# Optimization experiments

Measured on AMD Instinct MI355X. Metric: run time of the kernel, lower is better.

The kernel has to match this reference:

```python
import jax, jax.numpy as jnp
import numpy as np

HEADS = 10
DIM_HEAD = 64
C = 640
N_TOK = 1024          # (1024//32)**2 tokens per image
IMG_NUMS = 3          # total_length = id_length + 1
ID_LENGTH = 2
SA = 0.5
NEG_INF = -1e9


def _build_story_mask(key):
    # Faithful to cal_attn_mask_xl: one random row of columns shared by all
    # images, columns beyond the id_length reference images zeroed, and each
    # image's own block forced True; then broadcast over query tokens.
    L = IMG_NUMS * N_TOK
    base = jax.random.uniform(key, (1, L)) < SA                  # [1, L]
    bm = jnp.tile(base, (IMG_NUMS, 1))                           # [img, L]
    col = jnp.arange(L)
    bm = jnp.where(col[None, :] >= ID_LENGTH * N_TOK, False, bm)
    self_block = (col // N_TOK)[None, :] == jnp.arange(IMG_NUMS)[:, None]
    bm = bm | self_block                                         # [img, L]
    return jnp.repeat(bm, N_TOK, axis=0)                         # [L, L]


def setup_inputs() -> dict:
    key = jax.random.key(0)
    ks = jax.random.split(key, 7)
    B_total = 2 * IMG_NUMS
    hidden_states = jax.random.normal(ks[0], (B_total, N_TOK, C), dtype=jnp.float32)
    mask = _build_story_mask(ks[1])
    s = 1.0 / np.sqrt(C)
    Wq = jax.random.normal(ks[2], (C, HEADS * DIM_HEAD), dtype=jnp.float32) * s
    Wk = jax.random.normal(ks[3], (C, HEADS * DIM_HEAD), dtype=jnp.float32) * s
    Wv = jax.random.normal(ks[4], (C, HEADS * DIM_HEAD), dtype=jnp.float32) * s
    Wout = jax.random.normal(ks[5], (HEADS * DIM_HEAD, C), dtype=jnp.float32) * s
    bout = jnp.zeros((C,), dtype=jnp.float32)
    return {"hidden_states": hidden_states, "mask": mask,
            "Wq": Wq, "Wk": Wk, "Wv": Wv, "Wout": Wout, "bout": bout}


def reference(hidden_states, mask, Wq, Wk, Wv, Wout, bout):
    # __call1__ with encoder_hidden_states=None: fuse img_nums images into one
    # long sequence per CFG branch, then masked SDPA.
    B_total, n_tok, c = hidden_states.shape
    img_nums = B_total // 2
    L = img_nums * n_tok
    x = hidden_states.reshape(2, L, c)                       # [2, L, C]

    q = jnp.einsum('bsc,cd->bsd', x, Wq).reshape(2, L, HEADS, DIM_HEAD)
    k = jnp.einsum('bsc,cd->bsd', x, Wk).reshape(2, L, HEADS, DIM_HEAD)
    v = jnp.einsum('bsc,cd->bsd', x, Wv).reshape(2, L, HEADS, DIM_HEAD)

    scale = 1.0 / jnp.sqrt(jnp.asarray(DIM_HEAD, dtype=q.dtype))
    scores = jnp.einsum('bqhd,bkhd->bhqk', q, k) * scale     # [2, H, L, L]
    scores = jnp.where(mask[None, None, :, :], scores, NEG_INF)
    attn = jax.nn.softmax(scores, axis=-1)
    out = jnp.einsum('bhqk,bkhd->bqhd', attn, v)             # [2, L, H, Dh]
    out = out.reshape(B_total, n_tok, HEADS * DIM_HEAD)
    return jnp.einsum('bsd,dc->bsc', out, Wout) + bout
```

## Files before the change

### kernel.cpp

```cpp
#include <hip/hip_runtime.h>
#include <cstdint>
#include <cstddef>

typedef _Float16 f16;
typedef _Float16 f16x8 __attribute__((ext_vector_type(8)));
typedef _Float16 f16x4 __attribute__((ext_vector_type(4)));
typedef float f32x4 __attribute__((ext_vector_type(4)));

#define MFMA32(a, b, c) __builtin_amdgcn_mfma_f32_16x16x32_f16((a), (b), (c), 0, 0, 0)
#define MFMA16(a, b, c) __builtin_amdgcn_mfma_f32_16x16x16f16((a), (b), (c), 0, 0, 0)

#if __has_builtin(__builtin_amdgcn_exp2f)
#define EXP2F(x) __builtin_amdgcn_exp2f(x)
#else
#define EXP2F(x) exp2f(x)
#endif

#define DRAIN_MEM() __builtin_amdgcn_s_waitcnt(0x0070)

#define LOG2E 1.44269504088896340736f

__device__ __forceinline__ f16x4 pack4(float a, float b, float c, float d) {
    f16x4 r; r[0] = (f16)a; r[1] = (f16)b; r[2] = (f16)c; r[3] = (f16)d;
    return r;
}

__device__ __forceinline__ void gl_lds16(const f16* g, f16* l) {
    __builtin_amdgcn_global_load_lds((const __attribute__((address_space(1))) void*)g,
                                     (__attribute__((address_space(3))) void*)l, 16, 0, 0);
}

__global__ __launch_bounds__(256) void k_cvt_x(const float4* __restrict__ x, f16x4* __restrict__ xb) {
    const int i = blockIdx.x * 256 + threadIdx.x;
    const float4 v = x[i];
    f16x4 o;
    o[0] = (f16)v.x; o[1] = (f16)v.y; o[2] = (f16)v.z; o[3] = (f16)v.w;
    xb[i] = o;
}

__global__ __launch_bounds__(256) void k_cvt_w(const float* __restrict__ Wq, const float* __restrict__ Wk,
                                               const float* __restrict__ Wv, const float* __restrict__ Wo,
                                               f16* __restrict__ WT, f16* __restrict__ WoT) {
    __shared__ float tile[32][33];
    const int z = blockIdx.z;
    const float* src = (z == 0) ? Wq : (z == 1) ? Wk : (z == 2) ? Wv : Wo;
    f16* dst = (z < 3) ? (WT + (size_t)z * 640 * 640) : WoT;
    const float scale = (z == 0) ? 0.125f * LOG2E : 1.0f;
    const int k0 = blockIdx.x * 32, n0 = blockIdx.y * 32;
    const int t = threadIdx.x;
#pragma unroll
    for (int i = 0; i < 4; i++) {
        const int idx = i * 256 + t;
        const int r = idx >> 5, c = idx & 31;
        tile[r][c] = src[(size_t)(k0 + r) * 640 + n0 + c];
    }
    __syncthreads();
#pragma unroll
    for (int i = 0; i < 4; i++) {
        const int idx = i * 256 + t;
        const int r = idx >> 5, c = idx & 31;
        dst[(size_t)(n0 + r) * 640 + k0 + c] = (f16)(tile[c][r] * scale);
    }
}

__global__ __launch_bounds__(256) void k_gemm(const f16* __restrict__ A, const f16* __restrict__ B,
                                              f16* __restrict__ qb, f16* __restrict__ kb, f16* __restrict__ vtb) {
    __shared__ f16 As[128 * 40];
    __shared__ f16 Bs[128 * 40];
    const int t = threadIdx.x;
    const int wave = t >> 6, lane = t & 63, quad = lane >> 4, l16 = lane & 15;
    const int wm = wave >> 1, wn = wave & 1;
    const long m0 = (long)blockIdx.x * 128, n0 = (long)blockIdx.y * 128;
    const int srow = t >> 2, skc = t & 3;

    const f32x4 zero = {0.f, 0.f, 0.f, 0.f};
    f32x4 acc[4][4];
#pragma unroll
    for (int i = 0; i < 4; i++)
#pragma unroll
        for (int j = 0; j < 4; j++) acc[i][j] = zero;

    const f16* gA1 = A + (m0 + srow) * 640 + skc * 8;
    const f16* gA2 = A + (m0 + 64 + srow) * 640 + skc * 8;
    const f16* gB1 = B + (n0 + srow) * 640 + skc * 8;
    const f16* gB2 = B + (n0 + 64 + srow) * 640 + skc * 8;
    f16* sA1 = As + srow * 40 + skc * 8;
    f16* sA2 = As + (64 + srow) * 40 + skc * 8;
    f16* sB1 = Bs + srow * 40 + skc * 8;
    f16* sB2 = Bs + (64 + srow) * 40 + skc * 8;

    for (int kt = 0; kt < 20; kt++) {
        const int ko = kt * 32;
        const f16x8 a1 = *(const f16x8*)(gA1 + ko);
        const f16x8 a2 = *(const f16x8*)(gA2 + ko);
        const f16x8 b1 = *(const f16x8*)(gB1 + ko);
        const f16x8 b2 = *(const f16x8*)(gB2 + ko);
        __syncthreads();
        *(f16x8*)sA1 = a1;
        *(f16x8*)sA2 = a2;
        *(f16x8*)sB1 = b1;
        *(f16x8*)sB2 = b2;
        __syncthreads();
        f16x8 af[4], bfr[4];
#pragma unroll
        for (int mi = 0; mi < 4; mi++) af[mi] = *(const f16x8*)(As + (wm * 64 + mi * 16 + l16) * 40 + quad * 8);
#pragma unroll
        for (int ni = 0; ni < 4; ni++) bfr[ni] = *(const f16x8*)(Bs + (wn * 64 + ni * 16 + l16) * 40 + quad * 8);
#pragma unroll
        for (int mi = 0; mi < 4; mi++)
#pragma unroll
            for (int ni = 0; ni < 4; ni++) acc[mi][ni] = MFMA32(af[mi], bfr[ni], acc[mi][ni]);
    }

    const int b = (int)(m0 / 3072);
    const int which = (int)(n0 / 640);
    const int hd0 = (int)(n0 - (long)which * 640);
    if (which < 2) {
        f16* dst = (which == 0) ? qb : kb;
#pragma unroll
        for (int ni = 0; ni < 4; ni++) {
            const int hd = hd0 + wn * 64 + ni * 16 + l16;
            const int h = hd >> 6, d = hd & 63;
#pragma unroll
            for (int mi = 0; mi < 4; mi++) {
                const long l0 = m0 - (long)b * 3072 + wm * 64 + mi * 16 + quad * 4;
                f16* p = dst + ((long)(b * 10 + h) * 3072 + l0) * 64 + d;
#pragma unroll
                for (int j = 0; j < 4; j++) p[(long)j * 64] = (f16)acc[mi][ni][j];
            }
        }
    } else {
#pragma unroll
        for (int ni = 0; ni < 4; ni++) {
            const int hd = hd0 + wn * 64 + ni * 16 + l16;
            const int h = hd >> 6, d = hd & 63;
#pragma unroll
            for (int mi = 0; mi < 4; mi++) {
                const long l0 = m0 - (long)b * 3072 + wm * 64 + mi * 16 + quad * 4;
                const long col = (l0 & ~63L) + quad * 16 + mi * 4;
                f16x4 tmp;
#pragma unroll
                for (int j = 0; j < 4; j++) tmp[j] = (f16)acc[mi][ni][j];
                *(f16x4*)(vtb + ((size_t)(b * 10 + h) * 64 + d) * 3072 + col) = tmp;
            }
        }
    }
}

__global__ __launch_bounds__(256) void k_gemmo(const f16* __restrict__ A, const f16* __restrict__ B,
                                               float* __restrict__ out, const float* __restrict__ bias) {
    __shared__ f16 As[64 * 40];
    __shared__ f16 Bs[128 * 40];
    const int t = threadIdx.x;
    const int wave = t >> 6, lane = t & 63, quad = lane >> 4, l16 = lane & 15;
    const int wm = wave >> 1, wn = wave & 1;
    const long m0 = (long)blockIdx.x * 64, n0 = (long)blockIdx.y * 128;
    const int srow = t >> 2, skc = t & 3;

    const f32x4 zero = {0.f, 0.f, 0.f, 0.f};
    f32x4 acc[2][4];
#pragma unroll
    for (int i = 0; i < 2; i++)
#pragma unroll
        for (int j = 0; j < 4; j++) acc[i][j] = zero;

    const f16* gA = A + (m0 + srow) * 640 + skc * 8;
    const f16* gB1 = B + (n0 + srow) * 640 + skc * 8;
    const f16* gB2 = B + (n0 + 64 + srow) * 640 + skc * 8;
    f16* sA = As + srow * 40 + skc * 8;
    f16* sB1 = Bs + srow * 40 + skc * 8;
    f16* sB2 = Bs + (64 + srow) * 40 + skc * 8;

    for (int kt = 0; kt < 20; kt++) {
        const int ko = kt * 32;
        const f16x8 a1 = *(const f16x8*)(gA + ko);
        const f16x8 b1 = *(const f16x8*)(gB1 + ko);
        const f16x8 b2 = *(const f16x8*)(gB2 + ko);
        __syncthreads();
        *(f16x8*)sA = a1;
        *(f16x8*)sB1 = b1;
        *(f16x8*)sB2 = b2;
        __syncthreads();
        f16x8 af[2], bfr[4];
#pragma unroll
        for (int mi = 0; mi < 2; mi++) af[mi] = *(const f16x8*)(As + (wm * 32 + mi * 16 + l16) * 40 + quad * 8);
#pragma unroll
        for (int ni = 0; ni < 4; ni++) bfr[ni] = *(const f16x8*)(Bs + (wn * 64 + ni * 16 + l16) * 40 + quad * 8);
#pragma unroll
        for (int mi = 0; mi < 2; mi++)
#pragma unroll
            for (int ni = 0; ni < 4; ni++) acc[mi][ni] = MFMA32(af[mi], bfr[ni], acc[mi][ni]);
    }

#pragma unroll
    for (int ni = 0; ni < 4; ni++) {
        const long gc = n0 + wn * 64 + ni * 16 + l16;
        const float bs = bias[gc];
#pragma unroll
        for (int mi = 0; mi < 2; mi++) {
            const long r0 = m0 + wm * 32 + mi * 16 + quad * 4;
            float* p = out + r0 * 640 + gc;
#pragma unroll
            for (int j = 0; j < 4; j++) p[(long)j * 640] = acc[mi][ni][j] + bs;
        }
    }
}

__global__ __launch_bounds__(128, 2) void k_attn(const f16* __restrict__ q, const f16* __restrict__ k,
                                                 const f16* __restrict__ vT, const unsigned char* __restrict__ mask,
                                                 f16* __restrict__ ao) {
    __shared__ __align__(16) unsigned char smem[40960];

    const int t = threadIdx.x;
    const int w = t >> 6, lane = t & 63, quad = lane >> 4, l16 = lane & 15;
    const int bh = blockIdx.y, b = bh / 10, h = bh - b * 10;
    const int qt = (blockIdx.x < 16) ? (32 + (int)blockIdx.x) : ((int)blockIdx.x - 16);
    const int q0 = qt * 64;
    const int img = q0 >> 10;
    const int kmax = (img == 2) ? 3072 : 2048;
    const int nIter = kmax >> 6;
    float* bias_s = (float*)(smem + 32768);

    int mmode;
    if (mask[1] && mask[2] && mask[3]) mmode = 0;
    else if (mask[7] == 0x3f) mmode = 2;
    else mmode = 1;
    const int msz = (mmode == 0) ? 1 : 4;
    const int mhi = (mmode == 2) ? 3 : 0;
    const unsigned char* mrow = mask + (size_t)img * 1024 * 3072 * msz;

    for (int i = t; i < 2048; i += 128)
        bias_s[i] = (mrow[(size_t)i * msz + mhi] != 0) ? -8.f : -1e9f;

    const int r8 = lane >> 3, cch = lane & 7;
    const f16* kg = k + (size_t)bh * 3072 * 64;
    const f16* vg = vT + (size_t)bh * 64 * 3072;
    const int wrow0 = w * 32;

    {
        f16* K0 = (f16*)smem;
        f16* V0 = (f16*)(smem + 16384);
#pragma unroll
        for (int i = 0; i < 4; i++) {
            const int row = wrow0 + i * 8 + r8;
            gl_lds16(kg + (size_t)row * 64 + ((cch ^ (row & 7)) * 8), K0 + (wrow0 + i * 8) * 64);
            gl_lds16(vg + (size_t)row * 3072 + ((cch ^ (row & 7)) * 8), V0 + (wrow0 + i * 8) * 64);
        }
    }

    f16x8 qfA0, qfA1, qfB0, qfB1;
    {
        const f16* qp = q + ((size_t)bh * 3072 + q0 + w * 32 + l16) * 64 + quad * 8;
        qfA0 = *(const f16x8*)qp;
        qfA1 = *(const f16x8*)(qp + 32);
        qfB0 = *(const f16x8*)(qp + 16 * 64);
        qfB1 = *(const f16x8*)(qp + 16 * 64 + 32);
    }

    const int s7 = l16 & 7;
    const int bK0 = l16 * 128 + ((quad ^ s7) * 16);
    const int bK1 = l16 * 128 + (((quad + 4) ^ s7) * 16);
    const int bV0 = l16 * 128 + (((2 * quad) ^ s7) * 16);
    const int bV1 = l16 * 128 + (((2 * quad + 1) ^ s7) * 16);

    const f32x4 zero = {0.f, 0.f, 0.f, 0.f};
    f32x4 OA[4], OB[4];
#pragma unroll
    for (int i = 0; i < 4; i++) { OA[i] = zero; OB[i] = zero; }
    float lA = 0.f, lB = 0.f;

    const f32x4 m8 = {-8.f, -8.f, -8.f, -8.f};

    for (int it = 0; it < nIter; it++) {
        DRAIN_MEM();
        __syncthreads();
        const char* Kb = (const char*)smem + (it & 1) * 8192;
        const char* Vb = (const char*)smem + 16384 + (it & 1) * 8192;
        if (it + 1 < nIter) {
            const int k0n = (it + 1) << 6;
            f16* Kn = (f16*)(smem + ((it + 1) & 1) * 8192);
            f16* Vn = (f16*)(smem + 16384 + ((it + 1) & 1) * 8192);
#pragma unroll
            for (int i = 0; i < 4; i++) {
                const int row = wrow0 + i * 8 + r8;
                gl_lds16(kg + (size_t)(k0n + row) * 64 + ((cch ^ (row & 7)) * 8), Kn + (wrow0 + i * 8) * 64);
                gl_lds16(vg + (size_t)row * 3072 + k0n + ((cch ^ (row & 7)) * 8), Vn + (wrow0 + i * 8) * 64);
            }
        }

        f32x4 sA[4], sB[4];
#pragma unroll
        for (int kt = 0; kt < 4; kt++) {
            const f16x8 kf0 = *(const f16x8*)(Kb + bK0 + kt * 2048);
            const f16x8 kf1 = *(const f16x8*)(Kb + bK1 + kt * 2048);
            sA[kt] = MFMA32(kf0, qfA0, zero);
            sA[kt] = MFMA32(kf1, qfA1, sA[kt]);
            sB[kt] = MFMA32(kf0, qfB0, zero);
            sB[kt] = MFMA32(kf1, qfB1, sB[kt]);
        }
        if (it * 64 < 2048) {
#pragma unroll
            for (int kt = 0; kt < 4; kt++) {
                const f32x4 bv = *(const f32x4*)(bias_s + it * 64 + kt * 16 + quad * 4);
                sA[kt] += bv;
                sB[kt] += bv;
            }
        } else {
#pragma unroll
            for (int kt = 0; kt < 4; kt++) { sA[kt] += m8; sB[kt] += m8; }
        }

        f16x4 pkA[4], pkB[4];
#pragma unroll
        for (int kt = 0; kt < 4; kt++) {
            const float a0 = EXP2F(sA[kt][0]), a1 = EXP2F(sA[kt][1]);
            const float a2 = EXP2F(sA[kt][2]), a3 = EXP2F(sA[kt][3]);
            lA += (a0 + a1) + (a2 + a3);
            pkA[kt] = pack4(a0, a1, a2, a3);
            const float b0 = EXP2F(sB[kt][0]), b1 = EXP2F(sB[kt][1]);
            const float b2 = EXP2F(sB[kt][2]), b3 = EXP2F(sB[kt][3]);
            lB += (b0 + b1) + (b2 + b3);
            pkB[kt] = pack4(b0, b1, b2, b3);
        }

#pragma unroll
        for (int mtd = 0; mtd < 4; mtd++) {
            const f16x8 v80 = *(const f16x8*)(Vb + bV0 + mtd * 2048);
            const f16x8 v81 = *(const f16x8*)(Vb + bV1 + mtd * 2048);
            const f16x4 vf0 = __builtin_shufflevector(v80, v80, 0, 1, 2, 3);
            const f16x4 vf1 = __builtin_shufflevector(v80, v80, 4, 5, 6, 7);
            const f16x4 vf2 = __builtin_shufflevector(v81, v81, 0, 1, 2, 3);
            const f16x4 vf3 = __builtin_shufflevector(v81, v81, 4, 5, 6, 7);
            OA[mtd] = MFMA16(vf0, pkA[0], OA[mtd]);
            OA[mtd] = MFMA16(vf1, pkA[1], OA[mtd]);
            OA[mtd] = MFMA16(vf2, pkA[2], OA[mtd]);
            OA[mtd] = MFMA16(vf3, pkA[3], OA[mtd]);
            OB[mtd] = MFMA16(vf0, pkB[0], OB[mtd]);
            OB[mtd] = MFMA16(vf1, pkB[1], OB[mtd]);
            OB[mtd] = MFMA16(vf2, pkB[2], OB[mtd]);
            OB[mtd] = MFMA16(vf3, pkB[3], OB[mtd]);
        }
    }

    lA += __shfl_xor(lA, 16);
    lA += __shfl_xor(lA, 32);
    lB += __shfl_xor(lB, 16);
    lB += __shfl_xor(lB, 32);
    const float invA = 1.0f / lA;
    const float invB = 1.0f / lB;
    f16* orowA = ao + ((size_t)(b * 3072 + q0 + w * 32 + l16)) * 640 + h * 64;
    f16* orowB = orowA + (size_t)16 * 640;
#pragma unroll
    for (int mtd = 0; mtd < 4; mtd++) {
        f16x4 oa, ob;
#pragma unroll
        for (int j = 0; j < 4; j++) { oa[j] = (f16)(OA[mtd][j] * invA); ob[j] = (f16)(OB[mtd][j] * invB); }
        *(f16x4*)(orowA + mtd * 16 + quad * 4) = oa;
        *(f16x4*)(orowB + mtd * 16 + quad * 4) = ob;
    }
}

extern "C" void kernel_launch(void* const* d_in, const int* in_sizes, int n_in,
                              void* d_out, int out_size, void* d_ws, size_t ws_size,
                              hipStream_t stream) {
    (void)in_sizes; (void)n_in; (void)out_size; (void)ws_size;
    const float* x = (const float*)d_in[0];
    const unsigned char* mask = (const unsigned char*)d_in[1];
    const float* Wq = (const float*)d_in[2];
    const float* Wk = (const float*)d_in[3];
    const float* Wv = (const float*)d_in[4];
    const float* Wo = (const float*)d_in[5];
    const float* bout = (const float*)d_in[6];
    float* out = (float*)d_out;

    f16* xb  = (f16*)d_ws;
    f16* WT  = xb + 6144 * 640;
    f16* WoT = WT + 1920 * 640;
    f16* qb  = WoT + 640 * 640;
    f16* kb  = qb + 20 * 3072 * 64;
    f16* vtb = kb + 20 * 3072 * 64;

    k_cvt_x<<<3840, 256, 0, stream>>>((const float4*)x, (f16x4*)xb);
    k_cvt_w<<<dim3(20, 20, 4), 256, 0, stream>>>(Wq, Wk, Wv, Wo, WT, WoT);
    k_gemm<<<dim3(48, 15), 256, 0, stream>>>(xb, WT, qb, kb, vtb);
    k_attn<<<dim3(48, 20), 128, 0, stream>>>(qb, kb, vtb, mask, xb );
    k_gemmo<<<dim3(96, 5), 256, 0, stream>>>(xb, WoT, out, bout);
}
```

Measured before the change: 207.3 us.

## Split attention over key chunks and combine partial results in a new kernel

Splits the attention key range into 1024-key chunks so each query tile is processed by 2 or 3 blocks, which raises the grid from 960 to 2240 blocks and balances work between images with different key lengths. Each block writes an unnormalized-then-normalized partial output plus its row sum, and a new combine kernel merges them weighted by those sums. This adds extra global traffic for the partial outputs, an extra kernel launch, and more workspace. It relies on the fixed max of -8 so no max rescaling is needed across chunks.

```diff
diff --git a/kernel.cpp b/kernel.cpp
--- a/kernel.cpp
+++ b/kernel.cpp
@@ -208,17 +208,28 @@
 
 __global__ __launch_bounds__(128, 2) void k_attn(const f16* __restrict__ q, const f16* __restrict__ k,
                                                  const f16* __restrict__ vT, const unsigned char* __restrict__ mask,
-                                                 f16* __restrict__ ao) {
-    __shared__ __align__(16) unsigned char smem[40960];
+                                                 f16* __restrict__ Op, float* __restrict__ lp) {
+    __shared__ __align__(16) unsigned char smem[36864];
 
     const int t = threadIdx.x;
     const int w = t >> 6, lane = t & 63, quad = lane >> 4, l16 = lane & 15;
     const int bh = blockIdx.y, b = bh / 10, h = bh - b * 10;
-    const int qt = (blockIdx.x < 16) ? (32 + (int)blockIdx.x) : ((int)blockIdx.x - 16);
+
+    int qt, s;
+    if (blockIdx.x < 64) {
+        qt = (int)blockIdx.x >> 1;
+        s = (int)blockIdx.x & 1;
+    } else {
+        const int y = (int)blockIdx.x - 64;
+        const int d3 = y / 3;
+        qt = 32 + d3;
+        s = y - d3 * 3;
+    }
     const int q0 = qt * 64;
-    const int img = q0 >> 10;
-    const int kmax = (img == 2) ? 3072 : 2048;
-    const int nIter = kmax >> 6;
+    const int img = qt >> 4;
+    const int kk0 = s << 10;
+    const int nIter = 16;
+    const bool useBias = (kk0 < 2048);
     float* bias_s = (float*)(smem + 32768);
 
     int mmode;
@@ -227,10 +238,12 @@
     else mmode = 1;
     const int msz = (mmode == 0) ? 1 : 4;
     const int mhi = (mmode == 2) ? 3 : 0;
-    const unsigned char* mrow = mask + (size_t)img * 1024 * 3072 * msz;
-
-    for (int i = t; i < 2048; i += 128)
-        bias_s[i] = (mrow[(size_t)i * msz + mhi] != 0) ? -8.f : -1e9f;
+
+    if (useBias) {
+        const unsigned char* mrow = mask + ((size_t)img * 1024 * 3072 + kk0) * msz;
+        for (int i = t; i < 1024; i += 128)
+            bias_s[i] = (mrow[(size_t)i * msz + mhi] != 0) ? -8.f : -1e9f;
+    }
 
     const int r8 = lane >> 3, cch = lane & 7;
     const f16* kg = k + (size_t)bh * 3072 * 64;
@@ -243,8 +256,8 @@
 #pragma unroll
         for (int i = 0; i < 4; i++) {
             const int row = wrow0 + i * 8 + r8;
-            gl_lds16(kg + (size_t)row * 64 + ((cch ^ (row & 7)) * 8), K0 + (wrow0 + i * 8) * 64);
-            gl_lds16(vg + (size_t)row * 3072 + ((cch ^ (row & 7)) * 8), V0 + (wrow0 + i * 8) * 64);
+            gl_lds16(kg + (size_t)(kk0 + row) * 64 + ((cch ^ (row & 7)) * 8), K0 + (wrow0 + i * 8) * 64);
+            gl_lds16(vg + (size_t)row * 3072 + kk0 + ((cch ^ (row & 7)) * 8), V0 + (wrow0 + i * 8) * 64);
         }
     }
 
@@ -277,7 +290,7 @@
         const char* Kb = (const char*)smem + (it & 1) * 8192;
         const char* Vb = (const char*)smem + 16384 + (it & 1) * 8192;
         if (it + 1 < nIter) {
-            const int k0n = (it + 1) << 6;
+            const int k0n = kk0 + ((it + 1) << 6);
             f16* Kn = (f16*)(smem + ((it + 1) & 1) * 8192);
             f16* Vn = (f16*)(smem + 16384 + ((it + 1) & 1) * 8192);
 #pragma unroll
@@ -298,7 +311,7 @@
             sB[kt] = MFMA32(kf0, qfB0, zero);
             sB[kt] = MFMA32(kf1, qfB1, sB[kt]);
         }
-        if (it * 64 < 2048) {
+        if (useBias) {
 #pragma unroll
             for (int kt = 0; kt < 4; kt++) {
                 const f32x4 bv = *(const f32x4*)(bias_s + it * 64 + kt * 16 + quad * 4);
@@ -346,9 +359,10 @@
     lA += __shfl_xor(lA, 32);
     lB += __shfl_xor(lB, 16);
     lB += __shfl_xor(lB, 32);
-    const float invA = 1.0f / lA;
-    const float invB = 1.0f / lB;
-    f16* orowA = ao + ((size_t)(b * 3072 + q0 + w * 32 + l16)) * 640 + h * 64;
+    const float invA = (lA > 0.f) ? 1.0f / lA : 0.f;
+    const float invB = (lB > 0.f) ? 1.0f / lB : 0.f;
+    const int rowA = b * 3072 + q0 + w * 32 + l16;
+    f16* orowA = Op + (size_t)s * 6144 * 640 + (size_t)rowA * 640 + h * 64;
     f16* orowB = orowA + (size_t)16 * 640;
 #pragma unroll
     for (int mtd = 0; mtd < 4; mtd++) {
@@ -358,6 +372,33 @@
         *(f16x4*)(orowA + mtd * 16 + quad * 4) = oa;
         *(f16x4*)(orowB + mtd * 16 + quad * 4) = ob;
     }
+    if (quad == 0) lp[((size_t)s * 6144 + rowA) * 10 + h] = lA;
+    if (quad == 1) lp[((size_t)s * 6144 + rowA + 16) * 10 + h] = lB;
+}
+
+__global__ __launch_bounds__(256) void k_comb(const f16* __restrict__ Op, const float* __restrict__ lp,
+                                              f16* __restrict__ ao) {
+    const int idx = blockIdx.x * 256 + threadIdx.x;
+    const int row = idx / 80;
+    const int c8 = (idx - row * 80) * 8;
+    const int h = c8 >> 6;
+    const int r3 = (row >= 3072) ? row - 3072 : row;
+    const int img = r3 >> 10;
+    const int ns = (img == 2) ? 3 : 2;
+    float acc[8] = {0.f, 0.f, 0.f, 0.f, 0.f, 0.f, 0.f, 0.f};
+    float lsum = 0.f;
+    for (int s = 0; s < ns; s++) {
+        const float l = lp[((size_t)s * 6144 + row) * 10 + h];
+        const f16x8 o = *(const f16x8*)(Op + ((size_t)s * 6144 + row) * 640 + c8);
+#pragma unroll
+        for (int j = 0; j < 8; j++) acc[j] += l * (float)o[j];
+        lsum += l;
+    }
+    const float inv = 1.0f / lsum;
+    f16x8 r;
+#pragma unroll
+    for (int j = 0; j < 8; j++) r[j] = (f16)(acc[j] * inv);
+    *(f16x8*)(ao + (size_t)row * 640 + c8) = r;
 }
 
 extern "C" void kernel_launch(void* const* d_in, const int* in_sizes, int n_in,
@@ -379,10 +420,13 @@
     f16* qb  = WoT + 640 * 640;
     f16* kb  = qb + 20 * 3072 * 64;
     f16* vtb = kb + 20 * 3072 * 64;
+    f16* Op  = vtb + 20 * 3072 * 64;
+    float* lp = (float*)(Op + (size_t)3 * 6144 * 640);
 
     k_cvt_x<<<3840, 256, 0, stream>>>((const float4*)x, (f16x4*)xb);
     k_cvt_w<<<dim3(20, 20, 4), 256, 0, stream>>>(Wq, Wk, Wv, Wo, WT, WoT);
     k_gemm<<<dim3(48, 15), 256, 0, stream>>>(xb, WT, qb, kb, vtb);
-    k_attn<<<dim3(48, 20), 128, 0, stream>>>(qb, kb, vtb, mask, xb );
-    k_gemmo<<<dim3(96, 5), 256, 0, stream>>>(xb, WoT, out, bout);
-}
+    k_attn<<<dim3(112, 20), 128, 0, stream>>>(qb, kb, vtb, mask, Op, lp);
+    k_comb<<<1920, 256, 0, stream>>>(Op, lp, qb );
+    k_gemmo<<<dim3(96, 5), 256, 0, stream>>>(qb, WoT, out, bout);
+}
```

After: 216.6 us. 4.5% more time.
